# Optimization experiments

Hardware: AMD Instinct MI355X
Metric: run time of the kernel (lower is better)

## Reference

```python
import jax, jax.numpy as jnp
import numpy as np

NEG_SLOPE = 0.2  # PyG GATConv default leaky_relu slope


def _gat_layer(x, W, att_src, att_dst, bias, src, dst, num_nodes, heads, out_c, concat):
    # x: [N, F_in] -> h: [N, H, C]
    h = (x @ W).reshape(num_nodes, heads, out_c)
    a_src = jnp.einsum('nhc,hc->nh', h, att_src)  # [N, H]
    a_dst = jnp.einsum('nhc,hc->nh', h, att_dst)  # [N, H]
    # edge (src -> dst): attention logit per edge/head
    e = jax.nn.leaky_relu(a_src[src] + a_dst[dst], NEG_SLOPE)  # [E, H]
    # softmax over edges sharing the same destination node
    m = jax.ops.segment_max(e, dst, num_segments=num_nodes)  # [N, H]
    m = jnp.where(jnp.isfinite(m), m, 0.0)
    ex = jnp.exp(e - m[dst])
    denom = jax.ops.segment_sum(ex, dst, num_segments=num_nodes)  # [N, H]
    alpha = ex / (denom[dst] + 1e-16)  # [E, H]
    # weighted scatter-add aggregation
    msg = h[src] * alpha[:, :, None]  # [E, H, C]
    out = jax.ops.segment_sum(msg, dst, num_segments=num_nodes)  # [N, H, C]
    if concat:
        out = out.reshape(num_nodes, heads * out_c)
    else:
        out = out.mean(axis=1)
    return out + bias


def _add_self_loops(edge_index, num_nodes):
    loop = jnp.arange(num_nodes, dtype=edge_index.dtype)
    src = jnp.concatenate([edge_index[0], loop])
    dst = jnp.concatenate([edge_index[1], loop])
    return src, dst


def setup_inputs() -> dict:
    key = jax.random.key(0)
    ks = jax.random.split(key, 9)
    N, F_in, E, H, C, OUT = 30000, 256, 300000, 8, 128, 64
    x = jax.random.normal(ks[0], (N, F_in), dtype=jnp.float32)
    edge_index = jax.random.randint(ks[1], (2, E), 0, N, dtype=jnp.int32)
    s1 = 1.0 / np.sqrt(F_in)
    s2 = 1.0 / np.sqrt(H * C)
    return {
        'x': x,
        'edge_index': edge_index,
        'W1': jax.random.normal(ks[2], (F_in, H * C), dtype=jnp.float32) * s1,
        'att_src1': jax.random.normal(ks[3], (H, C), dtype=jnp.float32) * s2,
        'att_dst1': jax.random.normal(ks[4], (H, C), dtype=jnp.float32) * s2,
        'b1': jnp.zeros((H * C,), dtype=jnp.float32),
        'W2': jax.random.normal(ks[5], (H * C, OUT), dtype=jnp.float32) * s2,
        'att_src2': jax.random.normal(ks[6], (1, OUT), dtype=jnp.float32) * 0.125,
        'att_dst2': jax.random.normal(ks[7], (1, OUT), dtype=jnp.float32) * 0.125,
        'b2': jnp.zeros((OUT,), dtype=jnp.float32),
    }


def reference(x, edge_index, W1, att_src1, att_dst1, b1, W2, att_src2, att_dst2, b2):
    N = x.shape[0]
    src, dst = _add_self_loops(edge_index, N)
    # dropout layers are identity in eval mode
    h = _gat_layer(x, W1, att_src1, att_dst1, b1, src, dst, N, 8, 128, True)
    h = jax.nn.elu(h)
    out = _gat_layer(h, W2, att_src2, att_dst2, b2, src, dst, N, 1, 64, False)
    return jax.nn.log_softmax(out, axis=-1)
```

## Files before the change

kernel.cpp:

```cpp
#include <hip/hip_runtime.h>
#include <math.h>

#define N_NODES 30000
#define F_IN 256
#define E_RAW 300000
#define E_TOT (E_RAW + N_NODES)
#define HEADS 8
#define CH 128
#define HC 1024
#define OUTC 64
#define NEG_SLOPE 0.2f
#define CAP 64

typedef __attribute__((ext_vector_type(8))) short bf16x8;
typedef __attribute__((ext_vector_type(4))) float f32x4;
typedef __attribute__((ext_vector_type(2))) float f32x2;

__device__ __forceinline__ float bf2f(unsigned short u) {
    return __uint_as_float(((unsigned)u) << 16);
}
__device__ __forceinline__ unsigned short f2bf(float f) {
    unsigned b = __float_as_uint(f);
    b += 0x7FFFu + ((b >> 16) & 1u);
    return (unsigned short)(b >> 16);
}
__device__ __forceinline__ void edge_sd(const int* __restrict__ ei, int e, int& s, int& d) {
    if (e < E_RAW) { s = ei[e]; d = ei[E_RAW + e]; }
    else           { s = e - E_RAW; d = s; }
}
__device__ __forceinline__ void async_cp16(const void* g, void* l) {
    __builtin_amdgcn_global_load_lds((const __attribute__((address_space(1))) void*)g,
                                     (__attribute__((address_space(3))) void*)l, 16, 0, 0);
}
__device__ __forceinline__ int slotP(int s) {
    return ((s >> 6) << 6) + ((s >> 2) & 15) + ((s & 3) << 4);
}
__device__ __forceinline__ void wave_sync() {
    __builtin_amdgcn_fence(__ATOMIC_ACQ_REL, "wavefront");
    __builtin_amdgcn_wave_barrier();
}

#define NB_CVTX (N_NODES * F_IN / 4 / 256)
#define NB_DEG  ((E_TOT + 255) / 256)
#define NB_W1T  ((F_IN * HC + 255) / 256)
#define NB_W2T  ((HC * OUTC + 255) / 256)
#define NB_PREP (NB_CVTX + NB_DEG + NB_W1T + NB_W2T)

__global__ __launch_bounds__(256)
void prep_kernel(const float* __restrict__ x, unsigned short* __restrict__ xb,
                 const float* __restrict__ W1, unsigned short* __restrict__ W1t,
                 const float* __restrict__ W2, unsigned short* __restrict__ W2t,
                 const int* __restrict__ ei, int* __restrict__ deg)
{
    const int b = blockIdx.x, t = threadIdx.x;
    if (b < NB_CVTX) {
        int i = b * 256 + t;
        const float4 v = reinterpret_cast<const float4*>(x)[i];
        ushort4 o;
        o.x = f2bf(v.x); o.y = f2bf(v.y); o.z = f2bf(v.z); o.w = f2bf(v.w);
        reinterpret_cast<ushort4*>(xb)[i] = o;
    } else if (b < NB_CVTX + NB_DEG) {
        int e = (b - NB_CVTX) * 256 + t;
        if (e < E_TOT) {
            int s, d; edge_sd(ei, e, s, d);
            atomicAdd(&deg[d], 1);
        }
    } else if (b < NB_CVTX + NB_DEG + NB_W1T) {
        int i = (b - NB_CVTX - NB_DEG) * 256 + t;
        if (i < F_IN * HC) {
            int k = i >> 10, n = i & (HC - 1);
            W1t[n * F_IN + k] = f2bf(W1[i]);
        }
    } else {
        int i = (b - NB_CVTX - NB_DEG - NB_W1T) * 256 + t;
        if (i < HC * OUTC) {
            int s = i >> 6, n = i & (OUTC - 1);
            W2t[n * HC + s] = f2bf(W2[slotP(s) * OUTC + n]);
        }
    }
}

__global__ __launch_bounds__(256)
void gemm1_mfma(const unsigned short* __restrict__ A,
                const unsigned short* __restrict__ Bt,
                unsigned* __restrict__ Cp,
                const float* __restrict__ att_src, const float* __restrict__ att_dst,
                float* __restrict__ a_src, float* __restrict__ a_dst, int M)
{
    __shared__ unsigned short Al[128 * 64];
    __shared__ unsigned short Bl[128 * 64];
    __shared__ float s_src[128][2];
    __shared__ float s_dst[128][2];
    const int tid  = threadIdx.x;
    const int wave = tid >> 6, lane = tid & 63;
    const int quad = lane >> 4, l16 = lane & 15;
    const int wr = (wave >> 1) * 64, wc = (wave & 1) * 64;
    const int row0 = blockIdx.y * 128;
    const int col0 = blockIdx.x * 128;

    f32x4 acc[4][4];
#pragma unroll
    for (int i = 0; i < 4; i++)
#pragma unroll
        for (int j = 0; j < 4; j++) acc[i][j] = (f32x4){0.f, 0.f, 0.f, 0.f};

    for (int k0 = 0; k0 < F_IN; k0 += 64) {
#pragma unroll
        for (int p = 0; p < 4; p++) {
            int idx = tid + 256 * p;
            int r = idx >> 3, q = idx & 7;
            async_cp16(A + (size_t)(row0 + r) * F_IN + k0 + ((q ^ (r & 7)) * 8),
                       Al + (size_t)(wave * 64 + 256 * p) * 8);
        }
#pragma unroll
        for (int p = 0; p < 4; p++) {
            int idx = tid + 256 * p;
            int r = idx >> 3, q = idx & 7;
            async_cp16(Bt + (size_t)(col0 + r) * F_IN + k0 + ((q ^ (r & 7)) * 8),
                       Bl + (size_t)(wave * 64 + 256 * p) * 8);
        }
        __syncthreads();
#pragma unroll
        for (int kh = 0; kh < 2; kh++) {
            const int cx = (kh * 4 + quad) ^ (l16 & 7);
            bf16x8 af[4], bg[4];
#pragma unroll
            for (int i = 0; i < 4; i++)
                af[i] = *reinterpret_cast<const bf16x8*>(Al + ((wr + i * 16 + l16) * 8 + cx) * 8);
#pragma unroll
            for (int j = 0; j < 4; j++)
                bg[j] = *reinterpret_cast<const bf16x8*>(Bl + ((wc + j * 16 + l16) * 8 + cx) * 8);
#pragma unroll
            for (int i = 0; i < 4; i++)
#pragma unroll
                for (int j = 0; j < 4; j++)
                    acc[i][j] = __builtin_amdgcn_mfma_f32_16x16x32_bf16(af[i], bg[j], acc[i][j], 0, 0, 0);
        }
        __syncthreads();
    }
    const int D = ((col0 + wc) >> 6) * 16 + l16;
#pragma unroll
    for (int i = 0; i < 4; i++) {
#pragma unroll
        for (int r = 0; r < 4; r++) {
            int row = row0 + wr + i * 16 + quad * 4 + r;
            if (row >= M) continue;
            int w8 = __builtin_amdgcn_cvt_pk_fp8_f32(acc[i][0][r], acc[i][1][r], 0, false);
            w8 = __builtin_amdgcn_cvt_pk_fp8_f32(acc[i][2][r], acc[i][3][r], w8, true);
            Cp[(size_t)row * 256 + D] = (unsigned)w8;
        }
    }
    const float* asv = att_src + blockIdx.x * CH;
    const float* adv = att_dst + blockIdx.x * CH;
    float av[4], dv[4];
#pragma unroll
    for (int j = 0; j < 4; j++) {
        av[j] = asv[wc + j * 16 + l16];
        dv[j] = adv[wc + j * 16 + l16];
    }
#pragma unroll
    for (int i = 0; i < 4; i++) {
#pragma unroll
        for (int r = 0; r < 4; r++) {
            float ps = 0.f, pd = 0.f;
#pragma unroll
            for (int j = 0; j < 4; j++) {
                float cc = acc[i][j][r];
                ps += cc * av[j];
                pd += cc * dv[j];
            }
#pragma unroll
            for (int o = 1; o < 16; o <<= 1) {
                ps += __shfl_xor(ps, o);
                pd += __shfl_xor(pd, o);
            }
            if (l16 == 0) {
                int lr = wr + i * 16 + quad * 4 + r;
                s_src[lr][wc >> 6] = ps;
                s_dst[lr][wc >> 6] = pd;
            }
        }
    }
    __syncthreads();
    if (tid < 128) {
        int row = row0 + tid;
        if (row < M) {
            a_src[row * 8 + blockIdx.x] = s_src[tid][0] + s_src[tid][1];
            a_dst[row * 8 + blockIdx.x] = s_dst[tid][0] + s_dst[tid][1];
        }
    }
}

__global__ __launch_bounds__(256)
void gemm2_mfma(const unsigned short* __restrict__ A,
                const unsigned short* __restrict__ Bt,
                unsigned short* __restrict__ C,
                const float* __restrict__ att_src2, const float* __restrict__ att_dst2,
                float* __restrict__ a_src2, float* __restrict__ a_dst2, int M)
{
    __shared__ unsigned short Al[64 * 64];
    __shared__ unsigned short Bl[64 * 64];
    const int tid  = threadIdx.x;
    const int wave = tid >> 6, lane = tid & 63;
    const int quad = lane >> 4, l16 = lane & 15;
    const int wr = wave * 16;
    const int row0 = blockIdx.x * 64;

    f32x4 acc[4];
#pragma unroll
    for (int j = 0; j < 4; j++) acc[j] = (f32x4){0.f, 0.f, 0.f, 0.f};

    for (int k0 = 0; k0 < HC; k0 += 64) {
#pragma unroll
        for (int p = 0; p < 2; p++) {
            int idx = tid + 256 * p;
            int r = idx >> 3, q = idx & 7;
            async_cp16(A + (size_t)(row0 + r) * HC + k0 + ((q ^ (r & 7)) * 8),
                       Al + (size_t)(wave * 64 + 256 * p) * 8);
        }
#pragma unroll
        for (int p = 0; p < 2; p++) {
            int idx = tid + 256 * p;
            int r = idx >> 3, q = idx & 7;
            async_cp16(Bt + (size_t)r * HC + k0 + ((q ^ (r & 7)) * 8),
                       Bl + (size_t)(wave * 64 + 256 * p) * 8);
        }
        __syncthreads();
#pragma unroll
        for (int kh = 0; kh < 2; kh++) {
            const int cx = (kh * 4 + quad) ^ (l16 & 7);
            bf16x8 af, bg[4];
            af = *reinterpret_cast<const bf16x8*>(Al + ((wr + l16) * 8 + cx) * 8);
#pragma unroll
            for (int j = 0; j < 4; j++)
                bg[j] = *reinterpret_cast<const bf16x8*>(Bl + ((j * 16 + l16) * 8 + cx) * 8);
#pragma unroll
            for (int j = 0; j < 4; j++)
                acc[j] = __builtin_amdgcn_mfma_f32_16x16x32_bf16(af, bg[j], acc[j], 0, 0, 0);
        }
        __syncthreads();
    }
    float av[4], dv[4];
#pragma unroll
    for (int j = 0; j < 4; j++) {
        av[j] = att_src2[j * 16 + l16];
        dv[j] = att_dst2[j * 16 + l16];
    }
#pragma unroll
    for (int r = 0; r < 4; r++) {
        int row = row0 + wr + quad * 4 + r;
        float ps = 0.f, pd = 0.f;
#pragma unroll
        for (int j = 0; j < 4; j++) {
            float cc = acc[j][r];
            int col = j * 16 + l16;
            if (row < M) C[(size_t)row * OUTC + col] = f2bf(cc);
            ps += cc * av[j];
            pd += cc * dv[j];
        }
#pragma unroll
        for (int o = 1; o < 16; o <<= 1) {
            ps += __shfl_xor(ps, o);
            pd += __shfl_xor(pd, o);
        }
        if (l16 == 0 && row < M) {
            a_src2[row] = ps;
            a_dst2[row] = pd;
        }
    }
}

__global__ __launch_bounds__(256)
void alloc_kernel(const int* __restrict__ deg, int* __restrict__ rowstart,
                  int* __restrict__ cursor, int* __restrict__ counter)
{
    int d = blockIdx.x * 256 + threadIdx.x;
    int lane = threadIdx.x & 63;
    int v = (d < N_NODES) ? deg[d] : 0;
    int x = v;
#pragma unroll
    for (int o = 1; o < 64; o <<= 1) {
        int y = __shfl_up(x, o);
        if (lane >= o) x += y;
    }
    int excl = x - v;
    int total = __shfl(x, 63);
    int base = 0;
    if (lane == 63) base = atomicAdd(counter, total);
    base = __shfl(base, 63);
    if (d < N_NODES) {
        rowstart[d] = base + excl;
        cursor[d]   = base + excl;
    }
}

__global__ void scatter_kernel(const int* __restrict__ ei, int* __restrict__ cursor,
                               int* __restrict__ csr_src)
{
    int e = blockIdx.x * 256 + threadIdx.x;
    if (e >= E_TOT) return;
    int s, d; edge_sd(ei, e, s, d);
    int pos = atomicAdd(&cursor[d], 1);
    csr_src[pos] = s;
}

__global__ __launch_bounds__(256)
void agg1_fused(const int* __restrict__ rowstart, const int* __restrict__ degv,
                const int* __restrict__ csr_src,
                const unsigned* __restrict__ h1p,
                const float* __restrict__ a_src1, const float* __restrict__ a_dst1,
                const float* __restrict__ b1, unsigned short* __restrict__ out1)
{
    const int t   = threadIdx.x;
    const int sub = t >> 6;
    const int tl  = t & 63;
    const int h   = tl >> 3;
    const int d   = blockIdx.x * 4 + sub;

    __shared__ float exps[4][CAP * 8];
    __shared__ int   srcs[4][CAP];

    const int start = rowstart[d];
    const int deg   = degv[d];

    const float adst = a_dst1[d * 8 + h];
    const uint4* __restrict__ h1v = reinterpret_cast<const uint4*>(h1p);

    float denom_part = 0.f;
    float acc[16];
#pragma unroll
    for (int k = 0; k < 16; k++) acc[k] = 0.f;

    for (int c0 = 0; c0 < deg; c0 += CAP) {
        const int cend = min(deg - c0, CAP);
        for (int c = (tl & 7); c < cend; c += 8) {
            int s = csr_src[start + c0 + c];
            if (h == 0) srcs[sub][c] = s;
            float a = a_src1[s * 8 + h] + adst;
            float v = a > 0.f ? a : NEG_SLOPE * a;
            float ex = __expf(v);
            exps[sub][c * 8 + h] = ex;
            denom_part += ex;
        }
        wave_sync();
        {
            int   s_cur = srcs[sub][0];
            float w_cur = exps[sub][h];
            uint4 u_cur = h1v[(size_t)s_cur * 64 + tl];
            for (int c = 0; c < cend; c++) {
                int   s_nxt = 0; float w_nxt = 0.f; uint4 u_nxt;
                if (c + 1 < cend) {
                    s_nxt = srcs[sub][c + 1];
                    w_nxt = exps[sub][(c + 1) * 8 + h];
                    u_nxt = h1v[(size_t)s_nxt * 64 + tl];
                }
#pragma unroll
                for (int dw = 0; dw < 4; dw++) {
                    unsigned wd = (&u_cur.x)[dw];
                    f32x2 lo = __builtin_amdgcn_cvt_pk_f32_fp8((int)wd, false);
                    f32x2 hi = __builtin_amdgcn_cvt_pk_f32_fp8((int)wd, true);
                    acc[dw * 4 + 0] += w_cur * lo.x;
                    acc[dw * 4 + 1] += w_cur * lo.y;
                    acc[dw * 4 + 2] += w_cur * hi.x;
                    acc[dw * 4 + 3] += w_cur * hi.y;
                }
                s_cur = s_nxt; w_cur = w_nxt; u_cur = u_nxt;
            }
        }
        wave_sync();
    }
#pragma unroll
    for (int o = 1; o < 8; o <<= 1) denom_part += __shfl_xor(denom_part, o);
    const float dinv = 1.f / (denom_part + 1e-16f);

    unsigned short ov[16];
#pragma unroll
    for (int e = 0; e < 16; e++) {
        float v = acc[e] * dinv + b1[slotP(16 * tl + e)];
        v = v > 0.f ? v : __expf(v) - 1.f;
        ov[e] = f2bf(v);
    }
    uint4* op = reinterpret_cast<uint4*>(out1 + (size_t)d * HC + 16 * tl);
    op[0] = *reinterpret_cast<uint4*>(&ov[0]);
    op[1] = *reinterpret_cast<uint4*>(&ov[8]);
}

__global__ __launch_bounds__(256)
void agg2_lsm(const int* __restrict__ rowstart, const int* __restrict__ degv,
              const int* __restrict__ csr_src,
              const unsigned short* __restrict__ h2,
              const float* __restrict__ a_src2, const float* __restrict__ a_dst2,
              const float* __restrict__ b2, float* __restrict__ out)
{
    const int t = threadIdx.x;
    const int sub  = t >> 6;
    const int lane = t & 63;
    const int eo   = lane >> 4;
    const int cq   = lane & 15;
    const int d = blockIdx.x * 4 + sub;

    __shared__ float exs[4][CAP];
    __shared__ int   ss[4][CAP];

    const int start = rowstart[d];
    const int deg   = degv[d];

    const float adst = a_dst2[d];
    const uint2* __restrict__ h2v = reinterpret_cast<const uint2*>(h2);
    float denom_part = 0.f;
    float ax = 0.f, ay = 0.f, az = 0.f, aw = 0.f;

    for (int c0 = 0; c0 < deg; c0 += CAP) {
        const int cend = min(deg - c0, CAP);
        for (int c = lane; c < cend; c += 64) {
            int s = csr_src[start + c0 + c];
            ss[sub][c] = s;
            float a = a_src2[s] + adst;
            float v = a > 0.f ? a : NEG_SLOPE * a;
            float ex = __expf(v);
            exs[sub][c] = ex;
            denom_part += ex;
        }
        wave_sync();
        {
            int   cc = eo;
            float w0 = (cc < cend) ? exs[sub][cc] : 0.f;
            int   s0 = (cc < cend) ? ss[sub][cc] : ss[sub][0];
            uint2 u0 = h2v[(size_t)s0 * 16 + cq];
            for (int c = 0; c + 4 < cend; c += 4) {
                int cc1 = c + 4 + eo;
                float w1 = (cc1 < cend) ? exs[sub][cc1] : 0.f;
                int   s1 = (cc1 < cend) ? ss[sub][cc1] : ss[sub][0];
                uint2 u1 = h2v[(size_t)s1 * 16 + cq];
                ax += w0 * __uint_as_float(u0.x << 16);
                ay += w0 * __uint_as_float(u0.x & 0xFFFF0000u);
                az += w0 * __uint_as_float(u0.y << 16);
                aw += w0 * __uint_as_float(u0.y & 0xFFFF0000u);
                w0 = w1; s0 = s1; u0 = u1;
            }
            ax += w0 * __uint_as_float(u0.x << 16);
            ay += w0 * __uint_as_float(u0.x & 0xFFFF0000u);
            az += w0 * __uint_as_float(u0.y << 16);
            aw += w0 * __uint_as_float(u0.y & 0xFFFF0000u);
        }
        wave_sync();
    }
    ax += __shfl_xor(ax, 16); ax += __shfl_xor(ax, 32);
    ay += __shfl_xor(ay, 16); ay += __shfl_xor(ay, 32);
    az += __shfl_xor(az, 16); az += __shfl_xor(az, 32);
    aw += __shfl_xor(aw, 16); aw += __shfl_xor(aw, 32);
#pragma unroll
    for (int o = 32; o > 0; o >>= 1) denom_part += __shfl_xor(denom_part, o);
    const float dinv = 1.f / (denom_part + 1e-16f);

    float4 bb = reinterpret_cast<const float4*>(b2)[cq];
    float v0 = ax * dinv + bb.x;
    float v1 = ay * dinv + bb.y;
    float v2 = az * dinv + bb.z;
    float v3 = aw * dinv + bb.w;
    float m = fmaxf(fmaxf(v0, v1), fmaxf(v2, v3));
#pragma unroll
    for (int o = 1; o < 16; o <<= 1) m = fmaxf(m, __shfl_xor(m, o));
    float ex = __expf(v0 - m) + __expf(v1 - m) + __expf(v2 - m) + __expf(v3 - m);
    float ssum = ex;
#pragma unroll
    for (int o = 1; o < 16; o <<= 1) ssum += __shfl_xor(ssum, o);
    if (eo == 0) {
        float lg = __logf(ssum);
        reinterpret_cast<float4*>(out + (size_t)d * OUTC)[cq] =
            make_float4(v0 - m - lg, v1 - m - lg, v2 - m - lg, v3 - m - lg);
    }
}

extern "C" void kernel_launch(void* const* d_in, const int* in_sizes, int n_in,
                              void* d_out, int out_size, void* d_ws, size_t ws_size,
                              hipStream_t stream)
{
    const float* x   = (const float*)d_in[0];
    const int*   ei  = (const int*)d_in[1];
    const float* W1  = (const float*)d_in[2];
    const float* as1 = (const float*)d_in[3];
    const float* ad1 = (const float*)d_in[4];
    const float* b1  = (const float*)d_in[5];
    const float* W2  = (const float*)d_in[6];
    const float* as2 = (const float*)d_in[7];
    const float* ad2 = (const float*)d_in[8];
    const float* b2  = (const float*)d_in[9];

    char* p = (char*)d_ws;
    auto alloc = [&](size_t bytes) { char* r = p; p += (bytes + 255) & ~(size_t)255; return r; };

    char* region0 = (char*)alloc((size_t)N_NODES * HC * 2);
    unsigned* h1p = (unsigned*)region0;

    char* region1 = (char*)alloc((size_t)N_NODES * HC * 2);
    unsigned short* out1 = (unsigned short*)region1;
    unsigned short* xb   = (unsigned short*)region1;
    unsigned short* W1t  = (unsigned short*)(region1 + (size_t)N_NODES * F_IN * 2 + 256);

    unsigned short* W2t = (unsigned short*)alloc((size_t)OUTC * HC * 2);

    float* a_src1   = (float*)alloc((size_t)N_NODES * HEADS * 4);
    float* a_dst1   = (float*)alloc((size_t)N_NODES * HEADS * 4);
    int*   deg      = (int*)alloc((size_t)(N_NODES + 1) * 4);
    int*   counter  = deg + N_NODES;
    int*   rowstart = (int*)alloc((size_t)N_NODES * 4);
    int*   cursor   = (int*)alloc((size_t)N_NODES * 4);
    int*   csr_src  = (int*)alloc((size_t)E_TOT * 4);

    char* q = region0;
    auto alias = [&](size_t bytes) { char* r = q; q += (bytes + 255) & ~(size_t)255; return r; };
    unsigned short* h2 = (unsigned short*)alias((size_t)N_NODES * OUTC * 2);
    float* a_src2  = (float*)alias((size_t)N_NODES * 4);
    float* a_dst2  = (float*)alias((size_t)N_NODES * 4);

    hipMemsetAsync(deg, 0, (size_t)(N_NODES + 1) * 4, stream);

    prep_kernel<<<NB_PREP, 256, 0, stream>>>(x, xb, W1, W1t, W2, W2t, ei, deg);

    alloc_kernel<<<(N_NODES + 255) / 256, 256, 0, stream>>>(deg, rowstart, cursor, counter);
    scatter_kernel<<<(E_TOT + 255) / 256, 256, 0, stream>>>(ei, cursor, csr_src);

    gemm1_mfma<<<dim3(HC / 128, (N_NODES + 127) / 128), 256, 0, stream>>>(
        xb, W1t, h1p, as1, ad1, a_src1, a_dst1, N_NODES);
    agg1_fused<<<N_NODES / 4, 256, 0, stream>>>(rowstart, deg, csr_src, h1p, a_src1, a_dst1, b1, out1);

    gemm2_mfma<<<(N_NODES + 63) / 64, 256, 0, stream>>>(
        out1, W2t, h2, as2, ad2, a_src2, a_dst2, N_NODES);
    agg2_lsm<<<N_NODES / 4, 256, 0, stream>>>(rowstart, deg, csr_src, h2, a_src2, a_dst2, b2, (float*)d_out);
}
```

Baseline: 259.0 us.

## Fuse CSR scatter into gemm1 launch, split agg1, enlarge gemm2 row tile

Folds the edge scatter that builds the CSR source list into the gemm1 launch as extra leading blocks, so the two independent stages share one grid and one fewer kernel launch. Layer-1 aggregation now runs as two half-size launches selected by a base node offset. The layer-2 GEMM tile grows from 64 to 128 rows per block so each block reuses the W2 tile over more rows. The split agg1 adds a launch without an obvious benefit, and the scatter blocks can contend with GEMM blocks for compute units.

```diff
diff --git a/kernel.cpp b/kernel.cpp
--- a/kernel.cpp
+++ b/kernel.cpp
@@ -16,9 +16,6 @@
 typedef __attribute__((ext_vector_type(4))) float f32x4;
 typedef __attribute__((ext_vector_type(2))) float f32x2;
 
-__device__ __forceinline__ float bf2f(unsigned short u) {
-    return __uint_as_float(((unsigned)u) << 16);
-}
 __device__ __forceinline__ unsigned short f2bf(float f) {
     unsigned b = __float_as_uint(f);
     b += 0x7FFFu + ((b >> 16) & 1u);
@@ -45,6 +42,7 @@
 #define NB_W1T  ((F_IN * HC + 255) / 256)
 #define NB_W2T  ((HC * OUTC + 255) / 256)
 #define NB_PREP (NB_CVTX + NB_DEG + NB_W1T + NB_W2T)
+#define NB_G1   (8 * ((N_NODES + 127) / 128))
 
 __global__ __launch_bounds__(256)
 void prep_kernel(const float* __restrict__ x, unsigned short* __restrict__ xb,
@@ -81,196 +79,6 @@
 }
 
 __global__ __launch_bounds__(256)
-void gemm1_mfma(const unsigned short* __restrict__ A,
-                const unsigned short* __restrict__ Bt,
-                unsigned* __restrict__ Cp,
-                const float* __restrict__ att_src, const float* __restrict__ att_dst,
-                float* __restrict__ a_src, float* __restrict__ a_dst, int M)
-{
-    __shared__ unsigned short Al[128 * 64];
-    __shared__ unsigned short Bl[128 * 64];
-    __shared__ float s_src[128][2];
-    __shared__ float s_dst[128][2];
-    const int tid  = threadIdx.x;
-    const int wave = tid >> 6, lane = tid & 63;
-    const int quad = lane >> 4, l16 = lane & 15;
-    const int wr = (wave >> 1) * 64, wc = (wave & 1) * 64;
-    const int row0 = blockIdx.y * 128;
-    const int col0 = blockIdx.x * 128;
-
-    f32x4 acc[4][4];
-#pragma unroll
-    for (int i = 0; i < 4; i++)
-#pragma unroll
-        for (int j = 0; j < 4; j++) acc[i][j] = (f32x4){0.f, 0.f, 0.f, 0.f};
-
-    for (int k0 = 0; k0 < F_IN; k0 += 64) {
-#pragma unroll
-        for (int p = 0; p < 4; p++) {
-            int idx = tid + 256 * p;
-            int r = idx >> 3, q = idx & 7;
-            async_cp16(A + (size_t)(row0 + r) * F_IN + k0 + ((q ^ (r & 7)) * 8),
-                       Al + (size_t)(wave * 64 + 256 * p) * 8);
-        }
-#pragma unroll
-        for (int p = 0; p < 4; p++) {
-            int idx = tid + 256 * p;
-            int r = idx >> 3, q = idx & 7;
-            async_cp16(Bt + (size_t)(col0 + r) * F_IN + k0 + ((q ^ (r & 7)) * 8),
-                       Bl + (size_t)(wave * 64 + 256 * p) * 8);
-        }
-        __syncthreads();
-#pragma unroll
-        for (int kh = 0; kh < 2; kh++) {
-            const int cx = (kh * 4 + quad) ^ (l16 & 7);
-            bf16x8 af[4], bg[4];
-#pragma unroll
-            for (int i = 0; i < 4; i++)
-                af[i] = *reinterpret_cast<const bf16x8*>(Al + ((wr + i * 16 + l16) * 8 + cx) * 8);
-#pragma unroll
-            for (int j = 0; j < 4; j++)
-                bg[j] = *reinterpret_cast<const bf16x8*>(Bl + ((wc + j * 16 + l16) * 8 + cx) * 8);
-#pragma unroll
-            for (int i = 0; i < 4; i++)
-#pragma unroll
-                for (int j = 0; j < 4; j++)
-                    acc[i][j] = __builtin_amdgcn_mfma_f32_16x16x32_bf16(af[i], bg[j], acc[i][j], 0, 0, 0);
-        }
-        __syncthreads();
-    }
-    const int D = ((col0 + wc) >> 6) * 16 + l16;
-#pragma unroll
-    for (int i = 0; i < 4; i++) {
-#pragma unroll
-        for (int r = 0; r < 4; r++) {
-            int row = row0 + wr + i * 16 + quad * 4 + r;
-            if (row >= M) continue;
-            int w8 = __builtin_amdgcn_cvt_pk_fp8_f32(acc[i][0][r], acc[i][1][r], 0, false);
-            w8 = __builtin_amdgcn_cvt_pk_fp8_f32(acc[i][2][r], acc[i][3][r], w8, true);
-            Cp[(size_t)row * 256 + D] = (unsigned)w8;
-        }
-    }
-    const float* asv = att_src + blockIdx.x * CH;
-    const float* adv = att_dst + blockIdx.x * CH;
-    float av[4], dv[4];
-#pragma unroll
-    for (int j = 0; j < 4; j++) {
-        av[j] = asv[wc + j * 16 + l16];
-        dv[j] = adv[wc + j * 16 + l16];
-    }
-#pragma unroll
-    for (int i = 0; i < 4; i++) {
-#pragma unroll
-        for (int r = 0; r < 4; r++) {
-            float ps = 0.f, pd = 0.f;
-#pragma unroll
-            for (int j = 0; j < 4; j++) {
-                float cc = acc[i][j][r];
-                ps += cc * av[j];
-                pd += cc * dv[j];
-            }
-#pragma unroll
-            for (int o = 1; o < 16; o <<= 1) {
-                ps += __shfl_xor(ps, o);
-                pd += __shfl_xor(pd, o);
-            }
-            if (l16 == 0) {
-                int lr = wr + i * 16 + quad * 4 + r;
-                s_src[lr][wc >> 6] = ps;
-                s_dst[lr][wc >> 6] = pd;
-            }
-        }
-    }
-    __syncthreads();
-    if (tid < 128) {
-        int row = row0 + tid;
-        if (row < M) {
-            a_src[row * 8 + blockIdx.x] = s_src[tid][0] + s_src[tid][1];
-            a_dst[row * 8 + blockIdx.x] = s_dst[tid][0] + s_dst[tid][1];
-        }
-    }
-}
-
-__global__ __launch_bounds__(256)
-void gemm2_mfma(const unsigned short* __restrict__ A,
-                const unsigned short* __restrict__ Bt,
-                unsigned short* __restrict__ C,
-                const float* __restrict__ att_src2, const float* __restrict__ att_dst2,
-                float* __restrict__ a_src2, float* __restrict__ a_dst2, int M)
-{
-    __shared__ unsigned short Al[64 * 64];
-    __shared__ unsigned short Bl[64 * 64];
-    const int tid  = threadIdx.x;
-    const int wave = tid >> 6, lane = tid & 63;
-    const int quad = lane >> 4, l16 = lane & 15;
-    const int wr = wave * 16;
-    const int row0 = blockIdx.x * 64;
-
-    f32x4 acc[4];
-#pragma unroll
-    for (int j = 0; j < 4; j++) acc[j] = (f32x4){0.f, 0.f, 0.f, 0.f};
-
-    for (int k0 = 0; k0 < HC; k0 += 64) {
-#pragma unroll
-        for (int p = 0; p < 2; p++) {
-            int idx = tid + 256 * p;
-            int r = idx >> 3, q = idx & 7;
-            async_cp16(A + (size_t)(row0 + r) * HC + k0 + ((q ^ (r & 7)) * 8),
-                       Al + (size_t)(wave * 64 + 256 * p) * 8);
-        }
-#pragma unroll
-        for (int p = 0; p < 2; p++) {
-            int idx = tid + 256 * p;
-            int r = idx >> 3, q = idx & 7;
-            async_cp16(Bt + (size_t)r * HC + k0 + ((q ^ (r & 7)) * 8),
-                       Bl + (size_t)(wave * 64 + 256 * p) * 8);
-        }
-        __syncthreads();
-#pragma unroll
-        for (int kh = 0; kh < 2; kh++) {
-            const int cx = (kh * 4 + quad) ^ (l16 & 7);
-            bf16x8 af, bg[4];
-            af = *reinterpret_cast<const bf16x8*>(Al + ((wr + l16) * 8 + cx) * 8);
-#pragma unroll
-            for (int j = 0; j < 4; j++)
-                bg[j] = *reinterpret_cast<const bf16x8*>(Bl + ((j * 16 + l16) * 8 + cx) * 8);
-#pragma unroll
-            for (int j = 0; j < 4; j++)
-                acc[j] = __builtin_amdgcn_mfma_f32_16x16x32_bf16(af, bg[j], acc[j], 0, 0, 0);
-        }
-        __syncthreads();
-    }
-    float av[4], dv[4];
-#pragma unroll
-    for (int j = 0; j < 4; j++) {
-        av[j] = att_src2[j * 16 + l16];
-        dv[j] = att_dst2[j * 16 + l16];
-    }
-#pragma unroll
-    for (int r = 0; r < 4; r++) {
-        int row = row0 + wr + quad * 4 + r;
-        float ps = 0.f, pd = 0.f;
-#pragma unroll
-        for (int j = 0; j < 4; j++) {
-            float cc = acc[j][r];
-            int col = j * 16 + l16;
-            if (row < M) C[(size_t)row * OUTC + col] = f2bf(cc);
-            ps += cc * av[j];
-            pd += cc * dv[j];
-        }
-#pragma unroll
-        for (int o = 1; o < 16; o <<= 1) {
-            ps += __shfl_xor(ps, o);
-            pd += __shfl_xor(pd, o);
-        }
-        if (l16 == 0 && row < M) {
-            a_src2[row] = ps;
-            a_dst2[row] = pd;
-        }
-    }
-}
-
-__global__ __launch_bounds__(256)
 void alloc_kernel(const int* __restrict__ deg, int* __restrict__ rowstart,
                   int* __restrict__ cursor, int* __restrict__ counter)
 {
@@ -294,14 +102,129 @@
     }
 }
 
-__global__ void scatter_kernel(const int* __restrict__ ei, int* __restrict__ cursor,
-                               int* __restrict__ csr_src)
-{
-    int e = blockIdx.x * 256 + threadIdx.x;
-    if (e >= E_TOT) return;
-    int s, d; edge_sd(ei, e, s, d);
-    int pos = atomicAdd(&cursor[d], 1);
-    csr_src[pos] = s;
+__global__ __launch_bounds__(256)
+void gemm1_sc(const unsigned short* __restrict__ A,
+              const unsigned short* __restrict__ Bt,
+              unsigned* __restrict__ Cp,
+              const float* __restrict__ att_src, const float* __restrict__ att_dst,
+              float* __restrict__ a_src, float* __restrict__ a_dst, int M,
+              const int* __restrict__ ei, int* __restrict__ cursor,
+              int* __restrict__ csr_src)
+{
+    __shared__ unsigned short Al[128 * 64];
+    __shared__ unsigned short Bl[128 * 64];
+    __shared__ float s_src[128][2];
+    __shared__ float s_dst[128][2];
+    const int vb = blockIdx.x;
+    if (vb < NB_DEG) {
+        int e = vb * 256 + threadIdx.x;
+        if (e < E_TOT) {
+            int s, d; edge_sd(ei, e, s, d);
+            int pos = atomicAdd(&cursor[d], 1);
+            csr_src[pos] = s;
+        }
+        return;
+    }
+    const int bx = (vb - NB_DEG) & 7;
+    const int by = (vb - NB_DEG) >> 3;
+    const int tid  = threadIdx.x;
+    const int wave = tid >> 6, lane = tid & 63;
+    const int quad = lane >> 4, l16 = lane & 15;
+    const int wr = (wave >> 1) * 64, wc = (wave & 1) * 64;
+    const int row0 = by * 128;
+    const int col0 = bx * 128;
+
+    f32x4 acc[4][4];
+#pragma unroll
+    for (int i = 0; i < 4; i++)
+#pragma unroll
+        for (int j = 0; j < 4; j++) acc[i][j] = (f32x4){0.f, 0.f, 0.f, 0.f};
+
+    for (int k0 = 0; k0 < F_IN; k0 += 64) {
+#pragma unroll
+        for (int p = 0; p < 4; p++) {
+            int idx = tid + 256 * p;
+            int r = idx >> 3, q = idx & 7;
+            async_cp16(A + (size_t)(row0 + r) * F_IN + k0 + ((q ^ (r & 7)) * 8),
+                       Al + (size_t)(wave * 64 + 256 * p) * 8);
+        }
+#pragma unroll
+        for (int p = 0; p < 4; p++) {
+            int idx = tid + 256 * p;
+            int r = idx >> 3, q = idx & 7;
+            async_cp16(Bt + (size_t)(col0 + r) * F_IN + k0 + ((q ^ (r & 7)) * 8),
+                       Bl + (size_t)(wave * 64 + 256 * p) * 8);
+        }
+        __syncthreads();
+#pragma unroll
+        for (int kh = 0; kh < 2; kh++) {
+            const int cx = (kh * 4 + quad) ^ (l16 & 7);
+            bf16x8 af[4], bg[4];
+#pragma unroll
+            for (int i = 0; i < 4; i++)
+                af[i] = *reinterpret_cast<const bf16x8*>(Al + ((wr + i * 16 + l16) * 8 + cx) * 8);
+#pragma unroll
+            for (int j = 0; j < 4; j++)
+                bg[j] = *reinterpret_cast<const bf16x8*>(Bl + ((wc + j * 16 + l16) * 8 + cx) * 8);
+#pragma unroll
+            for (int i = 0; i < 4; i++)
+#pragma unroll
+                for (int j = 0; j < 4; j++)
+                    acc[i][j] = __builtin_amdgcn_mfma_f32_16x16x32_bf16(af[i], bg[j], acc[i][j], 0, 0, 0);
+        }
+        __syncthreads();
+    }
+    const int D = ((col0 + wc) >> 6) * 16 + l16;
+#pragma unroll
+    for (int i = 0; i < 4; i++) {
+#pragma unroll
+        for (int r = 0; r < 4; r++) {
+            int row = row0 + wr + i * 16 + quad * 4 + r;
+            if (row >= M) continue;
+            int w8 = __builtin_amdgcn_cvt_pk_fp8_f32(acc[i][0][r], acc[i][1][r], 0, false);
+            w8 = __builtin_amdgcn_cvt_pk_fp8_f32(acc[i][2][r], acc[i][3][r], w8, true);
+            Cp[(size_t)row * 256 + D] = (unsigned)w8;
+        }
+    }
+    const float* asv = att_src + bx * CH;
+    const float* adv = att_dst + bx * CH;
+    float av[4], dv[4];
+#pragma unroll
+    for (int j = 0; j < 4; j++) {
+        av[j] = asv[wc + j * 16 + l16];
+        dv[j] = adv[wc + j * 16 + l16];
+    }
+#pragma unroll
+    for (int i = 0; i < 4; i++) {
+#pragma unroll
+        for (int r = 0; r < 4; r++) {
+            float ps = 0.f, pd = 0.f;
+#pragma unroll
+            for (int j = 0; j < 4; j++) {
+                float cc = acc[i][j][r];
+                ps += cc * av[j];
+                pd += cc * dv[j];
+            }
+#pragma unroll
+            for (int o = 1; o < 16; o <<= 1) {
+                ps += __shfl_xor(ps, o);
+                pd += __shfl_xor(pd, o);
+            }
+            if (l16 == 0) {
+                int lr = wr + i * 16 + quad * 4 + r;
+                s_src[lr][wc >> 6] = ps;
+                s_dst[lr][wc >> 6] = pd;
+            }
+        }
+    }
+    __syncthreads();
+    if (tid < 128) {
+        int row = row0 + tid;
+        if (row < M) {
+            a_src[row * 8 + bx] = s_src[tid][0] + s_src[tid][1];
+            a_dst[row * 8 + bx] = s_dst[tid][0] + s_dst[tid][1];
+        }
+    }
 }
 
 __global__ __launch_bounds__(256)
@@ -309,13 +232,14 @@
                 const int* __restrict__ csr_src,
                 const unsigned* __restrict__ h1p,
                 const float* __restrict__ a_src1, const float* __restrict__ a_dst1,
-                const float* __restrict__ b1, unsigned short* __restrict__ out1)
+                const float* __restrict__ b1, unsigned short* __restrict__ out1,
+                int base)
 {
     const int t   = threadIdx.x;
     const int sub = t >> 6;
     const int tl  = t & 63;
     const int h   = tl >> 3;
-    const int d   = blockIdx.x * 4 + sub;
+    const int d   = base + blockIdx.x * 4 + sub;
 
     __shared__ float exps[4][CAP * 8];
     __shared__ int   srcs[4][CAP];
@@ -383,6 +307,94 @@
     uint4* op = reinterpret_cast<uint4*>(out1 + (size_t)d * HC + 16 * tl);
     op[0] = *reinterpret_cast<uint4*>(&ov[0]);
     op[1] = *reinterpret_cast<uint4*>(&ov[8]);
+}
+
+__global__ __launch_bounds__(256)
+void gemm2_mfma(const unsigned short* __restrict__ A,
+                const unsigned short* __restrict__ Bt,
+                unsigned short* __restrict__ C,
+                const float* __restrict__ att_src2, const float* __restrict__ att_dst2,
+                float* __restrict__ a_src2, float* __restrict__ a_dst2, int M)
+{
+    __shared__ unsigned short Al[128 * 64];
+    __shared__ unsigned short Bl[64 * 64];
+    const int tid  = threadIdx.x;
+    const int wave = tid >> 6, lane = tid & 63;
+    const int quad = lane >> 4, l16 = lane & 15;
+    const int wr = wave * 32;
+    const int row0 = blockIdx.x * 128;
+
+    f32x4 acc[2][4];
+#pragma unroll
+    for (int i = 0; i < 2; i++)
+#pragma unroll
+        for (int j = 0; j < 4; j++) acc[i][j] = (f32x4){0.f, 0.f, 0.f, 0.f};
+
+    for (int k0 = 0; k0 < HC; k0 += 64) {
+#pragma unroll
+        for (int p = 0; p < 4; p++) {
+            int idx = tid + 256 * p;
+            int r = idx >> 3, q = idx & 7;
+            async_cp16(A + (size_t)(row0 + r) * HC + k0 + ((q ^ (r & 7)) * 8),
+                       Al + (size_t)(wave * 64 + 256 * p) * 8);
+        }
+#pragma unroll
+        for (int p = 0; p < 2; p++) {
+            int idx = tid + 256 * p;
+            int r = idx >> 3, q = idx & 7;
+            async_cp16(Bt + (size_t)r * HC + k0 + ((q ^ (r & 7)) * 8),
+                       Bl + (size_t)(wave * 64 + 256 * p) * 8);
+        }
+        __syncthreads();
+#pragma unroll
+        for (int kh = 0; kh < 2; kh++) {
+            const int cx = (kh * 4 + quad) ^ (l16 & 7);
+            bf16x8 af[2], bg[4];
+#pragma unroll
+            for (int i = 0; i < 2; i++)
+                af[i] = *reinterpret_cast<const bf16x8*>(Al + ((wr + i * 16 + l16) * 8 + cx) * 8);
+#pragma unroll
+            for (int j = 0; j < 4; j++)
+                bg[j] = *reinterpret_cast<const bf16x8*>(Bl + ((j * 16 + l16) * 8 + cx) * 8);
+#pragma unroll
+            for (int i = 0; i < 2; i++)
+#pragma unroll
+                for (int j = 0; j < 4; j++)
+                    acc[i][j] = __builtin_amdgcn_mfma_f32_16x16x32_bf16(af[i], bg[j], acc[i][j], 0, 0, 0);
+        }
+        __syncthreads();
+    }
+    float av[4], dv[4];
+#pragma unroll
+    for (int j = 0; j < 4; j++) {
+        av[j] = att_src2[j * 16 + l16];
+        dv[j] = att_dst2[j * 16 + l16];
+    }
+#pragma unroll
+    for (int i = 0; i < 2; i++) {
+#pragma unroll
+        for (int r = 0; r < 4; r++) {
+            int row = row0 + wr + i * 16 + quad * 4 + r;
+            float ps = 0.f, pd = 0.f;
+#pragma unroll
+            for (int j = 0; j < 4; j++) {
+                float cc = acc[i][j][r];
+                int col = j * 16 + l16;
+                if (row < M) C[(size_t)row * OUTC + col] = f2bf(cc);
+                ps += cc * av[j];
+                pd += cc * dv[j];
+            }
+#pragma unroll
+            for (int o = 1; o < 16; o <<= 1) {
+                ps += __shfl_xor(ps, o);
+                pd += __shfl_xor(pd, o);
+            }
+            if (l16 == 0 && row < M) {
+                a_src2[row] = ps;
+                a_dst2[row] = pd;
+            }
+        }
+    }
 }
 
 __global__ __launch_bounds__(256)
@@ -519,13 +531,14 @@
     prep_kernel<<<NB_PREP, 256, 0, stream>>>(x, xb, W1, W1t, W2, W2t, ei, deg);
 
     alloc_kernel<<<(N_NODES + 255) / 256, 256, 0, stream>>>(deg, rowstart, cursor, counter);
-    scatter_kernel<<<(E_TOT + 255) / 256, 256, 0, stream>>>(ei, cursor, csr_src);
-
-    gemm1_mfma<<<dim3(HC / 128, (N_NODES + 127) / 128), 256, 0, stream>>>(
-        xb, W1t, h1p, as1, ad1, a_src1, a_dst1, N_NODES);
-    agg1_fused<<<N_NODES / 4, 256, 0, stream>>>(rowstart, deg, csr_src, h1p, a_src1, a_dst1, b1, out1);
-
-    gemm2_mfma<<<(N_NODES + 63) / 64, 256, 0, stream>>>(
+
+    gemm1_sc<<<NB_DEG + NB_G1, 256, 0, stream>>>(
+        xb, W1t, h1p, as1, ad1, a_src1, a_dst1, N_NODES, ei, cursor, csr_src);
+
+    agg1_fused<<<N_NODES / 8, 256, 0, stream>>>(rowstart, deg, csr_src, h1p, a_src1, a_dst1, b1, out1, 0);
+    agg1_fused<<<N_NODES / 8, 256, 0, stream>>>(rowstart, deg, csr_src, h1p, a_src1, a_dst1, b1, out1, N_NODES / 2);
+
+    gemm2_mfma<<<(N_NODES + 127) / 128, 256, 0, stream>>>(
         out1, W2t, h2, as2, ad2, a_src2, a_dst2, N_NODES);
     agg2_lsm<<<N_NODES / 4, 256, 0, stream>>>(rowstart, deg, csr_src, h2, a_src2, a_dst2, b2, (float*)d_out);
 }
```

Result: slower. 269.7 us (+4.1%).
